# Performance work log

Hardware: AMD Instinct MI355X
Metric: run time of the kernel (lower is better)

The kernel has to match this reference:

```python
import jax, jax.numpy as jnp
import numpy as np

K = 10          # n_near
BN_EPS = 1e-5   # BatchNorm eps; running stats at init: mean=0, var=1


def knn_idx(xt, k):
    # xt: [b, n, c] -> [b, n, k] indices of k nearest (incl. self)
    sq = jnp.sum(xt * xt, axis=-1)                               # [b, n]
    d = sq[:, :, None] - 2.0 * jnp.einsum('bnc,bmc->bnm', xt, xt) + sq[:, None, :]
    return jax.lax.top_k(-d, k)[1]                               # [b, n, k]


def graph_feature(x, k):
    # x: [b, c, n] -> [b, 2c, n, k]  (DGCNN edge features)
    xt = x.transpose(0, 2, 1)                                    # [b, n, c]
    idx = knn_idx(xt, k)                                         # [b, n, k]
    nei = jnp.take_along_axis(xt[:, None, :, :], idx[..., None], axis=2)  # [b, n, k, c]
    cen = xt[:, :, None, :]                                      # [b, n, 1, c]
    feat = jnp.concatenate([nei - cen, jnp.broadcast_to(cen, nei.shape)], axis=-1)
    return feat.transpose(0, 3, 1, 2)                            # [b, 2c, n, k]


def conv_bn_act(x, w, b, g, t):
    # 1x1 conv (any spatial rank) + inference BatchNorm (mean=0, var=1) + GELU
    sh = (1, -1) + (1,) * (x.ndim - 2)
    y = jnp.einsum('oi,bi...->bo...', w, x) + b.reshape(sh)
    y = y * (g.reshape(sh) / jnp.sqrt(1.0 + BN_EPS)) + t.reshape(sh)
    return jax.nn.gelu(y)


def setup_inputs() -> dict:
    key = jax.random.key(0)
    ks = jax.random.split(key, 8)
    d = {'x': jax.random.normal(ks[0], (8, 64, 2048), jnp.float32)}
    dims = {'11': (152, 128), '12': (181, 152), '21': (430, 362),
            '22': (512, 430), '31': (595, 693), '32': (512, 595)}
    for i, (tag, (o, inp)) in enumerate(dims.items()):
        d['w' + tag] = jax.random.normal(jax.random.fold_in(key, i + 1), (o, inp), jnp.float32) * 0.02
        d['b' + tag] = jnp.zeros((o,), jnp.float32)
        d['g' + tag] = jnp.ones((o,), jnp.float32)
        d['t' + tag] = jnp.zeros((o,), jnp.float32)
    return d


def reference(x, w11, b11, g11, t11, w12, b12, g12, t12,
              w21, b21, g21, t21, w22, b22, g22, t22,
              w31, b31, g31, t31, w32, b32, g32, t32):
    f = graph_feature(x, K)                       # [b, 128, n, k]
    f = conv_bn_act(f, w11, b11, g11, t11)
    f = conv_bn_act(f, w12, b12, g12, t12)        # [b, 181, n, k]
    x1 = jnp.max(f, axis=-1)                      # [b, 181, n]
    f = graph_feature(x1, K)                      # [b, 362, n, k]
    f = conv_bn_act(f, w21, b21, g21, t21)
    f = conv_bn_act(f, w22, b22, g22, t22)        # [b, 512, n, k]
    x2 = jnp.max(f, axis=-1)                      # [b, 512, n]
    f = jnp.concatenate([x1, x2], axis=1)         # [b, 693, n]
    f = conv_bn_act(f, w31, b31, g31, t31)
    f = conv_bn_act(f, w32, b32, g32, t32)        # [b, 512, n]
    return f
```

## Files before the change

kernel.cpp:

```cpp
#include <hip/hip_runtime.h>


typedef float f4 __attribute__((ext_vector_type(4)));
typedef float f32x4 __attribute__((ext_vector_type(4)));
typedef short bf16x8 __attribute__((ext_vector_type(8)));

#define BNRSQ 0.9999950000374997f

__device__ __forceinline__ float gelu_f(float x){
  float a = 0.7978845608028654f * (x + 0.044715f * x * x * x);
  float e = __expf(2.0f * a);
  float t = 1.0f - 2.0f / (e + 1.0f);
  return 0.5f * x * (1.0f + t);
}

__device__ __forceinline__ short f2b(float x){
  unsigned u = __float_as_uint(x);
  unsigned r = (u + 0x7fffu + ((u >> 16) & 1u)) >> 16;
  return (short)r;
}
__device__ __forceinline__ float b2f(short s){
  return __uint_as_float(((unsigned)(unsigned short)s) << 16);
}

__global__ void makewt_k(const float* __restrict__ W, float* __restrict__ dst,
                         int O, int Cin, int Cpad, int ld, int split){
  int id = blockIdx.x * 256 + threadIdx.x;
  if (id >= Cpad * O) return;
  int c = id / O;
  int o = id - c * O;
  float v = 0.f;
  if (c < Cin){
    float w0 = W[(size_t)o * ld + c];
    v = split ? (W[(size_t)o * ld + Cin + c] - w0) : w0;
  }
  dst[id] = v;
}

__global__ void makew12r_k(const float* __restrict__ w12, float* __restrict__ Wr){
  int id = blockIdx.x * 256 + threadIdx.x;
  if (id >= 38 * 192 * 4) return;
  int i = id & 3;
  int c = (id >> 2) % 192;
  int kq = id / 768;
  int k = kq * 4 + i;
  float v = 0.f;
  if (c < 181 && k < 152) v = w12[(size_t)c * 152 + k];
  Wr[id] = v;
}

__global__ void makewsb_k(const float* __restrict__ W, short* __restrict__ dst){
  int n = blockIdx.x;
  int k = threadIdx.x;
  if (k >= 192) return;
  short v = 0;
  if (k < 181){
    if (n < 430) v = f2b(W[(size_t)n * 362 + k]);
    else if (n >= 448 && n < 878){
      int m = n - 448;
      v = f2b(W[(size_t)m * 362 + 181 + k] - W[(size_t)m * 362 + k]);
    }
  }
  dst[(size_t)n * 192 + k] = v;
}

__global__ void makewb_k(const float* __restrict__ W, short* __restrict__ dst,
                         int N, int K, int Kpad){
  int n = blockIdx.y;
  int k = blockIdx.x * 256 + threadIdx.x;
  if (k >= Kpad) return;
  short v = 0;
  if (n < N && k < K) v = f2b(W[(size_t)n * K + k]);
  dst[(size_t)n * Kpad + k] = v;
}

__global__ __launch_bounds__(256) void transpose_k(const float* __restrict__ x, float* __restrict__ xt){
  __shared__ float tile[64][65];
  int b = blockIdx.y;
  int n0 = blockIdx.x * 64;
  int t = threadIdx.x;
  int a = t & 63, r = t >> 6;
  #pragma unroll
  for (int s = 0; s < 16; s++){
    int c = r + s * 4;
    tile[c][a] = x[((size_t)b * 64 + c) * 2048 + n0 + a];
  }
  __syncthreads();
  #pragma unroll
  for (int s = 0; s < 16; s++){
    int n = r + s * 4;
    xt[((size_t)b * 2048 + n0 + n) * 64 + a] = tile[a][n];
  }
}

__global__ __launch_bounds__(256) void sqnorm_k(const float* __restrict__ X, float* __restrict__ sq,
                                                int C, int ld, int npts){
  int gid = blockIdx.x * blockDim.x + threadIdx.x;
  int wid = gid >> 6, lane = gid & 63;
  if (wid >= npts) return;
  const float* row = X + (size_t)wid * ld;
  float s = 0.f;
  for (int c = lane; c < C; c += 64){ float v = row[c]; s += v * v; }
  #pragma unroll
  for (int off = 32; off; off >>= 1) s += __shfl_xor(s, off);
  if (lane == 0) sq[wid] = s;
}

__global__ __launch_bounds__(256) void dist_k(const float* __restrict__ X, const float* __restrict__ sq,
                                              float* __restrict__ dist, int C, int ldx){
  __shared__ float As[16][132];
  __shared__ float Bs[16][132];
  const int z = blockIdx.z;
  const float* Xb = X + (size_t)z * 2048 * ldx;
  const float* sqb = sq + (z << 11);
  float* db = dist + (size_t)z * 2048 * 2048;
  const int i0 = blockIdx.y * 128, j0 = blockIdx.x * 128;
  const int t = threadIdx.x;
  const int ti = t >> 4, tj = t & 15;
  const int r = t & 127, q8 = (t >> 7) * 8;
  float acc[2][2][4][4];
  #pragma unroll
  for (int a = 0; a < 2; a++)
    #pragma unroll
    for (int b = 0; b < 2; b++)
      #pragma unroll
      for (int u = 0; u < 4; u++)
        #pragma unroll
        for (int v = 0; v < 4; v++) acc[a][b][u][v] = 0.f;
  const float* Ag = Xb + (size_t)(i0 + r) * ldx + q8;
  const float* Bg = Xb + (size_t)(j0 + r) * ldx + q8;
  for (int c0 = 0; c0 < C; c0 += 16){
    f4 av0 = *(const f4*)(Ag + c0);
    f4 av1 = *(const f4*)(Ag + c0 + 4);
    f4 bv0 = *(const f4*)(Bg + c0);
    f4 bv1 = *(const f4*)(Bg + c0 + 4);
    __syncthreads();
    #pragma unroll
    for (int i = 0; i < 4; i++){
      As[q8 + i][r] = av0[i];  As[q8 + 4 + i][r] = av1[i];
      Bs[q8 + i][r] = bv0[i];  Bs[q8 + 4 + i][r] = bv1[i];
    }
    __syncthreads();
    #pragma unroll
    for (int k = 0; k < 16; k++){
      f4 a0 = *(const f4*)&As[k][ti * 4];
      f4 a1 = *(const f4*)&As[k][ti * 4 + 64];
      f4 b0 = *(const f4*)&Bs[k][tj * 4];
      f4 b1 = *(const f4*)&Bs[k][tj * 4 + 64];
      #pragma unroll
      for (int u = 0; u < 4; u++)
        #pragma unroll
        for (int v = 0; v < 4; v++){
          acc[0][0][u][v] += a0[u] * b0[v];
          acc[0][1][u][v] += a0[u] * b1[v];
          acc[1][0][u][v] += a1[u] * b0[v];
          acc[1][1][u][v] += a1[u] * b1[v];
        }
    }
  }
  #pragma unroll
  for (int ia = 0; ia < 2; ia++){
    #pragma unroll
    for (int u = 0; u < 4; u++){
      int i = i0 + ia * 64 + ti * 4 + u;
      float si = sqb[i];
      #pragma unroll
      for (int jb = 0; jb < 2; jb++){
        int j = j0 + jb * 64 + tj * 4;
        f4 o;
        #pragma unroll
        for (int v = 0; v < 4; v++) o[v] = si + sqb[j + v] - 2.0f * acc[ia][jb][u][v];
        *(f4*)&db[(size_t)i * 2048 + j] = o;
      }
    }
  }
}

__global__ __launch_bounds__(256) void topk_k(const float* __restrict__ dist, int* __restrict__ idxout){
  int z = blockIdx.y;
  int lane = threadIdx.x & 63;
  int row = blockIdx.x * 4 + (threadIdx.x >> 6);
  const float* d = dist + (size_t)z * 2048 * 2048 + (size_t)row * 2048;
  float v[32];
  #pragma unroll
  for (int s = 0; s < 32; s++) v[s] = d[s * 64 + lane];
  int* outp = idxout + (size_t)z * 20480 + (size_t)row * 10;
  for (int it = 0; it < 10; ++it){
    float bv = 3.0e38f; int bi = 0x7fffffff;
    #pragma unroll
    for (int s = 0; s < 32; s++){
      if (v[s] < bv){ bv = v[s]; bi = s * 64 + lane; }
    }
    #pragma unroll
    for (int off = 32; off; off >>= 1){
      float ov = __shfl_xor(bv, off);
      int   oi = __shfl_xor(bi, off);
      if (ov < bv || (ov == bv && oi < bi)){ bv = ov; bi = oi; }
    }
    #pragma unroll
    for (int s = 0; s < 32; s++) if (s * 64 + lane == bi) v[s] = 3.0e38f;
    if (lane == 0) outp[it] = bi;
  }
}

__global__ __launch_bounds__(256) void yz_k(const float* __restrict__ Amat, int C,
                                            const float* __restrict__ B1, const float* __restrict__ B2,
                                            int O, float* __restrict__ Y, float* __restrict__ Z){
  __shared__ float As[16][68];
  __shared__ float B1s[16][68];
  __shared__ float B2s[16][68];
  int m0 = blockIdx.y * 64, o0 = blockIdx.x * 64;
  int t = threadIdx.x;
  int cc = t & 15, rr = t >> 4;
  int oo = t & 63, kk = t >> 6;
  float accY[4][4], accZ[4][4];
  #pragma unroll
  for (int u = 0; u < 4; u++)
    #pragma unroll
    for (int v = 0; v < 4; v++){ accY[u][v] = 0.f; accZ[u][v] = 0.f; }
  for (int c0 = 0; c0 < C; c0 += 16){
    #pragma unroll
    for (int u = 0; u < 4; u++){
      int ii = rr + u * 16;
      As[cc][ii] = ((c0 + cc) < C) ? Amat[(size_t)(m0 + ii) * C + c0 + cc] : 0.f;
    }
    #pragma unroll
    for (int u = 0; u < 4; u++){
      int c = kk * 4 + u;
      bool ok = ((c0 + c) < C) && ((o0 + oo) < O);
      B1s[c][oo] = ok ? B1[(size_t)(c0 + c) * O + o0 + oo] : 0.f;
      B2s[c][oo] = ok ? B2[(size_t)(c0 + c) * O + o0 + oo] : 0.f;
    }
    __syncthreads();
    #pragma unroll
    for (int k = 0; k < 16; k++){
      f4 a  = *(const f4*)&As[k][rr * 4];
      f4 b1 = *(const f4*)&B1s[k][cc * 4];
      f4 b2 = *(const f4*)&B2s[k][cc * 4];
      #pragma unroll
      for (int u = 0; u < 4; u++)
        #pragma unroll
        for (int v = 0; v < 4; v++){
          accY[u][v] += a[u] * b1[v];
          accZ[u][v] += a[u] * b2[v];
        }
    }
    __syncthreads();
  }
  #pragma unroll
  for (int u = 0; u < 4; u++){
    int m = m0 + rr * 4 + u;
    #pragma unroll
    for (int v = 0; v < 4; v++){
      int o = o0 + cc * 4 + v;
      if (o < O){
        Y[(size_t)m * O + o] = accY[u][v];
        Z[(size_t)m * O + o] = accZ[u][v];
      }
    }
  }
}

__global__ __launch_bounds__(256) void fused1_k(
    const float* __restrict__ Y1, const float* __restrict__ Z1,
    const int* __restrict__ idx, const float* __restrict__ Wr12,
    const float* __restrict__ bb11, const float* __restrict__ gg11, const float* __restrict__ tt11,
    const float* __restrict__ bb12, const float* __restrict__ gg12, const float* __restrict__ tt12,
    float* __restrict__ x1t){
  __shared__ float h1[80][152];
  __shared__ int sidx[80];
  const int n0 = blockIdx.x * 8;
  const int t = threadIdx.x;
  if (t < 80) sidx[t] = idx[(size_t)n0 * 10 + t];
  __syncthreads();
  const int base = (n0 >> 11) << 11;
  {
    const int tc = t & 63, tr = t >> 6;
    for (int c = tc; c < 152; c += 64){
      float bb = bb11[c], sc = gg11[c] * BNRSQ, tb = tt11[c];
      for (int r = tr; r < 80; r += 4){
        int p = r / 10;
        int j = base + sidx[r];
        float y = Y1[(size_t)j * 152 + c] + Z1[(size_t)(n0 + p) * 152 + c];
        h1[r][c] = gelu_f((y + bb) * sc + tb);
      }
    }
  }
  __syncthreads();
  const int p = t >> 5, kh = (t >> 4) & 1, cg = t & 15;
  const int rbase = p * 10 + kh * 5;
  #pragma unroll 1
  for (int jh = 0; jh < 2; jh++){
    float acc[5][6];
    #pragma unroll
    for (int k = 0; k < 5; k++)
      #pragma unroll
      for (int j = 0; j < 6; j++) acc[k][j] = 0.f;
    for (int kq = 0; kq < 38; kq++){
      const float* wp = Wr12 + ((size_t)kq * 192 + cg) * 4 + jh * 6 * 64;
      f4 wv[6];
      #pragma unroll
      for (int j = 0; j < 6; j++) wv[j] = *(const f4*)(wp + j * 64);
      f4 hv[5];
      #pragma unroll
      for (int k = 0; k < 5; k++) hv[k] = *(const f4*)&h1[rbase + k][kq * 4];
      #pragma unroll
      for (int k = 0; k < 5; k++)
        #pragma unroll
        for (int j = 0; j < 6; j++)
          acc[k][j] += hv[k][0] * wv[j][0] + hv[k][1] * wv[j][1]
                     + hv[k][2] * wv[j][2] + hv[k][3] * wv[j][3];
    }
    #pragma unroll
    for (int j = 0; j < 6; j++){
      int c = cg + (jh * 6 + j) * 16;
      float m = 0.f;
      if (c < 181){
        float bb = bb12[c], sc = gg12[c] * BNRSQ, tb = tt12[c];
        m = -3.0e38f;
        #pragma unroll
        for (int k = 0; k < 5; k++){
          float v = gelu_f((acc[k][j] + bb) * sc + tb);
          m = fmaxf(m, v);
        }
      }
      float o = __shfl_xor(m, 16);
      m = fmaxf(m, o);
      if (kh == 0) x1t[(size_t)(n0 + p) * 192 + c] = (c < 181) ? m : 0.f;
    }
  }
}

__global__ __launch_bounds__(256) void castx1_k(const float* __restrict__ x1t, short* __restrict__ x1b){
  int id = blockIdx.x * 256 + threadIdx.x;
  f4 v = *(const f4*)&x1t[(size_t)id * 4];
  short4 o;
  o.x = f2b(v[0]); o.y = f2b(v[1]); o.z = f2b(v[2]); o.w = f2b(v[3]);
  *(short4*)&x1b[(size_t)id * 4] = o;
}

__global__ __launch_bounds__(256) void h2_k(
    const float* __restrict__ YZ, const int* __restrict__ idx,
    const float* __restrict__ bb21, const float* __restrict__ gg21, const float* __restrict__ tt21,
    short* __restrict__ H2){
  __shared__ int sidx[10];
  int bl = blockIdx.x;
  int t = threadIdx.x;
  if (t < 10) sidx[t] = ((bl >> 11) << 11) + idx[(size_t)bl * 10 + t];
  __syncthreads();
  int cA = t;
  int cB = t + 256;
  float zA = YZ[(size_t)bl * 896 + 448 + cA] + bb21[cA];
  float scA = gg21[cA] * BNRSQ, tbA = tt21[cA];
  float zB = 0.f, scB = 0.f, tbB = 0.f;
  bool realB = cB < 430, padB = cB < 448;
  if (realB){
    zB = YZ[(size_t)bl * 896 + 448 + cB] + bb21[cB];
    scB = gg21[cB] * BNRSQ; tbB = tt21[cB];
  }
  #pragma unroll
  for (int k = 0; k < 10; k++){
    int nb = sidx[k];
    size_t rb = ((size_t)bl * 10 + k) * 448;
    float yA = YZ[(size_t)nb * 896 + cA] + zA;
    H2[rb + cA] = f2b(gelu_f(yA * scA + tbA));
    if (padB){
      short v = 0;
      if (realB){
        float yB = YZ[(size_t)nb * 896 + cB] + zB;
        v = f2b(gelu_f(yB * scB + tbB));
      }
      H2[rb + cB] = v;
    }
  }
}

template<int MODE>
__global__ __launch_bounds__(256) void gemm_k(const short* __restrict__ A,
                                              const short* __restrict__ Bt,
                                              int Kp, int Nld, int Nreal,
                                              const float* __restrict__ bv,
                                              const float* __restrict__ gv,
                                              const float* __restrict__ tv,
                                              void* __restrict__ outp){
  __shared__ short As[128][40];
  __shared__ short Bs[128][40];
  const int t = threadIdx.x;
  const int w = t >> 6, l = t & 63;
  const int m0 = blockIdx.y * 128, n0 = blockIdx.x * 128;
  f32x4 acc[2][8];
  #pragma unroll
  for (int i = 0; i < 2; i++)
    #pragma unroll
    for (int j = 0; j < 8; j++) acc[i][j] = (f32x4)0.f;
  const int ar = t >> 2, akc = t & 3;
  const short* Ag0 = A + (size_t)(m0 + ar) * Kp + akc * 8;
  const short* Ag1 = A + (size_t)(m0 + 64 + ar) * Kp + akc * 8;
  const short* Bg0 = Bt + (size_t)(n0 + ar) * Kp + akc * 8;
  const short* Bg1 = Bt + (size_t)(n0 + 64 + ar) * Kp + akc * 8;
  const int mrow = w * 32 + (l & 15);
  const int kg = (l >> 4) * 8;
  const int cl = l & 15;
  for (int k0 = 0; k0 < Kp; k0 += 32){
    int4 va0 = *(const int4*)(Ag0 + k0);
    int4 va1 = *(const int4*)(Ag1 + k0);
    int4 vb0 = *(const int4*)(Bg0 + k0);
    int4 vb1 = *(const int4*)(Bg1 + k0);
    __syncthreads();
    *(int4*)&As[ar][akc * 8]      = va0;
    *(int4*)&As[ar + 64][akc * 8] = va1;
    *(int4*)&Bs[ar][akc * 8]      = vb0;
    *(int4*)&Bs[ar + 64][akc * 8] = vb1;
    __syncthreads();
    bf16x8 a0 = *(const bf16x8*)&As[mrow][kg];
    bf16x8 a1 = *(const bf16x8*)&As[mrow + 16][kg];
    #pragma unroll
    for (int ni = 0; ni < 8; ni++){
      bf16x8 b = *(const bf16x8*)&Bs[cl + ni * 16][kg];
      acc[0][ni] = __builtin_amdgcn_mfma_f32_16x16x32_bf16(a0, b, acc[0][ni], 0, 0, 0);
      acc[1][ni] = __builtin_amdgcn_mfma_f32_16x16x32_bf16(a1, b, acc[1][ni], 0, 0, 0);
    }
  }
  const int rbase = (l >> 4) * 4;
  #pragma unroll
  for (int ni = 0; ni < 8; ni++){
    int n = n0 + ni * 16 + cl;
    float bb = 0.f, sc = 0.f, tb = 0.f;
    if (MODE != 2 && n < Nreal){ bb = bv[n]; sc = gv[n] * BNRSQ; tb = tv[n]; }
    #pragma unroll
    for (int mi = 0; mi < 2; mi++){
      #pragma unroll
      for (int r = 0; r < 4; r++){
        int m = m0 + w * 32 + mi * 16 + rbase + r;
        float a = acc[mi][ni][r];
        float v = (MODE == 2) ? a : gelu_f((a + bb) * sc + tb);
        if (MODE == 0) ((short*)outp)[(size_t)m * Nld + n] = f2b(v);
        else           ((float*)outp)[(size_t)m * Nld + n] = v;
      }
    }
  }
}

__global__ __launch_bounds__(256) void kmax_k(const short* __restrict__ Pb, short* __restrict__ x2b){
  int p = blockIdx.x;
  int t = threadIdx.x;
  #pragma unroll
  for (int j = 0; j < 2; j++){
    int o = t + j * 256;
    float m = -3.0e38f;
    #pragma unroll
    for (int k = 0; k < 10; k++) m = fmaxf(m, b2f(Pb[((size_t)p * 10 + k) * 512 + o]));
    x2b[(size_t)p * 512 + o] = f2b(m);
  }
}

__global__ __launch_bounds__(256) void fcat_k(const float* __restrict__ x1t, const short* __restrict__ x2b,
                                              short* __restrict__ F){
  size_t g = blockIdx.x;
  int t = threadIdx.x;
  for (int c = t; c < 704; c += 256){
    short v = 0;
    if (c < 181) v = f2b(x1t[g * 192 + c]);
    else if (c < 693) v = x2b[g * 512 + (c - 181)];
    F[g * 704 + c] = v;
  }
}

__global__ __launch_bounds__(256) void trout_k(const float* __restrict__ H6, float* __restrict__ out){
  __shared__ float tile[64][65];
  int b = blockIdx.z;
  int nc = blockIdx.x * 64, oc = blockIdx.y * 64;
  int t = threadIdx.x;
  int a = t & 63, r = t >> 6;
  #pragma unroll
  for (int s = 0; s < 16; s++){
    int nl = r + s * 4;
    tile[nl][a] = H6[((size_t)b * 2048 + nc + nl) * 512 + oc + a];
  }
  __syncthreads();
  #pragma unroll
  for (int s = 0; s < 16; s++){
    int ol = r + s * 4;
    out[((size_t)(b * 512 + oc + ol)) * 2048 + nc + a] = tile[a][ol];
  }
}

extern "C" void kernel_launch(void* const* d_in, const int* in_sizes, int n_in,
                              void* d_out, int out_size, void* d_ws, size_t ws_size,
                              hipStream_t stream) {
  const float* x   = (const float*)d_in[0];
  const float* w11 = (const float*)d_in[1];
  const float* b11 = (const float*)d_in[2];
  const float* g11 = (const float*)d_in[3];
  const float* t11 = (const float*)d_in[4];
  const float* w12 = (const float*)d_in[5];
  const float* b12 = (const float*)d_in[6];
  const float* g12 = (const float*)d_in[7];
  const float* t12 = (const float*)d_in[8];
  const float* w21 = (const float*)d_in[9];
  const float* b21 = (const float*)d_in[10];
  const float* g21 = (const float*)d_in[11];
  const float* t21 = (const float*)d_in[12];
  const float* w22 = (const float*)d_in[13];
  const float* b22 = (const float*)d_in[14];
  const float* g22 = (const float*)d_in[15];
  const float* t22 = (const float*)d_in[16];
  const float* w31 = (const float*)d_in[17];
  const float* b31 = (const float*)d_in[18];
  const float* g31 = (const float*)d_in[19];
  const float* t31 = (const float*)d_in[20];
  const float* w32 = (const float*)d_in[21];
  const float* b32 = (const float*)d_in[22];
  const float* g32 = (const float*)d_in[23];
  const float* t32 = (const float*)d_in[24];
  float* out = (float*)d_out;
  char* ws = (char*)d_ws;

  size_t off = 0;
  auto alloc = [&](size_t nbytes) -> char* {
    char* p = ws + off;
    off += ((nbytes + 255) & ~(size_t)255);
    return p;
  };
  float* x1t  = (float*)alloc((size_t)16384 * 192 * 4);
  short* x1b  = (short*)alloc((size_t)16384 * 192 * 2);
  short* x2b  = (short*)alloc((size_t)16384 * 512 * 2);
  float* sq1  = (float*)alloc(65536);
  float* sq2  = (float*)alloc(65536);
  int*   idx1 = (int*)  alloc(655360);
  int*   idx2 = (int*)  alloc(655360);
  float* WaT11 = (float*)alloc(64 * 152 * 4);
  float* WdT11 = (float*)alloc(64 * 152 * 4);
  float* Wr12  = (float*)alloc(38 * 192 * 4 * 4);
  short* W21sb = (short*)alloc((size_t)896 * 192 * 2);
  short* W22b  = (short*)alloc((size_t)512 * 448 * 2);
  short* W31b  = (short*)alloc((size_t)640 * 704 * 2);
  short* W32b  = (short*)alloc((size_t)512 * 640 * 2);
  char* arena = ws + off;
  const size_t ARENA = 93323264;
  if (off + ARENA > ws_size) return;
  float* distP = (float*)(arena);
  float* Y1    = (float*)(arena + 67108864);
  float* Z1    = (float*)(arena + 77070336);
  float* xt    = (float*)(arena + 87031808);
  short* Pb    = (short*)(arena);
  short* H2b   = (short*)(arena + 41943040);
  float* YZ2g  = (float*)(arena + 78643200);
  short* F     = (short*)(arena);
  short* H5    = (short*)(arena + 23068672);
  float* H6    = (float*)(arena + 44040192);

  auto mk = [&](const float* W, float* dst, int O, int Cin, int Cpad, int ld, int split){
    int n = Cpad * O;
    makewt_k<<<dim3((n + 255) / 256), dim3(256), 0, stream>>>(W, dst, O, Cin, Cpad, ld, split);
  };
  mk(w11, WaT11, 152, 64, 64, 128, 0);
  mk(w11, WdT11, 152, 64, 64, 128, 1);
  makew12r_k<<<dim3(114), dim3(256), 0, stream>>>(w12, Wr12);
  makewsb_k<<<dim3(896), dim3(256), 0, stream>>>(w21, W21sb);
  makewb_k<<<dim3(2, 512), dim3(256), 0, stream>>>(w22, W22b, 512, 430, 448);
  makewb_k<<<dim3(3, 640), dim3(256), 0, stream>>>(w31, W31b, 595, 693, 704);
  makewb_k<<<dim3(3, 512), dim3(256), 0, stream>>>(w32, W32b, 512, 595, 640);

  transpose_k<<<dim3(32, 8), dim3(256), 0, stream>>>(x, xt);
  sqnorm_k<<<dim3(4096), dim3(256), 0, stream>>>(xt, sq1, 64, 64, 16384);

  for (int pb = 0; pb < 2; pb++){
    dist_k<<<dim3(16, 16, 4), dim3(256), 0, stream>>>(xt + (size_t)pb * 4 * 2048 * 64,
                                                      sq1 + pb * 8192, distP, 64, 64);
    topk_k<<<dim3(512, 4), dim3(256), 0, stream>>>(distP, idx1 + (size_t)pb * 4 * 20480);
  }
  yz_k<<<dim3(3, 256), dim3(256), 0, stream>>>(xt, 64, WaT11, WdT11, 152, Y1, Z1);
  fused1_k<<<dim3(2048), dim3(256), 0, stream>>>(Y1, Z1, idx1, Wr12,
                                                 b11, g11, t11, b12, g12, t12, x1t);
  castx1_k<<<dim3(3072), dim3(256), 0, stream>>>(x1t, x1b);
  sqnorm_k<<<dim3(4096), dim3(256), 0, stream>>>(x1t, sq2, 192, 192, 16384);

  for (int pb = 0; pb < 2; pb++){
    dist_k<<<dim3(16, 16, 4), dim3(256), 0, stream>>>(x1t + (size_t)pb * 4 * 2048 * 192,
                                                      sq2 + pb * 8192, distP, 192, 192);
    topk_k<<<dim3(512, 4), dim3(256), 0, stream>>>(distP, idx2 + (size_t)pb * 4 * 20480);
  }
  for (int g = 0; g < 4; g++){
    gemm_k<2><<<dim3(7, 32), dim3(256), 0, stream>>>(x1b + (size_t)g * 4096 * 192, W21sb,
                                                     192, 896, 896,
                                                     nullptr, nullptr, nullptr, (void*)YZ2g);
    h2_k<<<dim3(4096), dim3(256), 0, stream>>>(YZ2g, idx2 + (size_t)g * 40960,
                                               b21, g21, t21, H2b);
    gemm_k<0><<<dim3(4, 320), dim3(256), 0, stream>>>(H2b, W22b, 448, 512, 512,
                                                      b22, g22, t22, (void*)Pb);
    kmax_k<<<dim3(4096), dim3(256), 0, stream>>>(Pb, x2b + (size_t)g * 4096 * 512);
  }

  fcat_k<<<dim3(16384), dim3(256), 0, stream>>>(x1t, x2b, F);
  gemm_k<0><<<dim3(5, 128), dim3(256), 0, stream>>>(F, W31b, 704, 640, 595,
                                                    b31, g31, t31, (void*)H5);
  gemm_k<1><<<dim3(4, 128), dim3(256), 0, stream>>>(H5, W32b, 640, 512, 512,
                                                    b32, g32, t32, (void*)H6);
  trout_k<<<dim3(32, 8, 8), dim3(256), 0, stream>>>(H6, out);
}
```

Measured before the change: 1.112 ms.

## Fuse neighbor gather+GELU into conv22 GEMM and fold cast/sqnorm into fused1

Removes the h2_k kernel and its materialized bf16 H2 buffer. The conv22 GEMM now gathers Y/Z rows by kNN index, applies the layer-21 bias/BN/GELU in registers, and writes bf16 straight into LDS. fused1_k is restructured to handle 4 points per block with 32-wide channel groups, and now also emits the bf16 copy of x1 and its squared norms. This drops the castx1 and sqnorm launches. In exchange, the GEMM A-tile loads become scattered fp32 gathers with per-element GELU recomputed for each output-column tile, which adds ALU work and irregular memory traffic.

```diff
diff --git a/kernel.cpp b/kernel.cpp
--- a/kernel.cpp
+++ b/kernel.cpp
@@ -72,6 +72,15 @@
   short v = 0;
   if (n < N && k < K) v = f2b(W[(size_t)n * K + k]);
   dst[(size_t)n * Kpad + k] = v;
+}
+
+__global__ void makebnp_k(const float* __restrict__ b21, const float* __restrict__ g21,
+                          const float* __restrict__ t21, float* __restrict__ bnp){
+  int c = blockIdx.x * 256 + threadIdx.x;
+  if (c >= 448) return;
+  float bb = 0.f, sc = 0.f, tb = 0.f;
+  if (c < 430){ bb = b21[c]; sc = g21[c] * BNRSQ; tb = t21[c]; }
+  bnp[c] = bb; bnp[448 + c] = sc; bnp[896 + c] = tb;
 }
 
 __global__ __launch_bounds__(256) void transpose_k(const float* __restrict__ x, float* __restrict__ xt){
@@ -266,19 +275,19 @@
     const int* __restrict__ idx, const float* __restrict__ Wr12,
     const float* __restrict__ bb11, const float* __restrict__ gg11, const float* __restrict__ tt11,
     const float* __restrict__ bb12, const float* __restrict__ gg12, const float* __restrict__ tt12,
-    float* __restrict__ x1t){
-  __shared__ float h1[80][152];
-  __shared__ int sidx[80];
-  const int n0 = blockIdx.x * 8;
+    float* __restrict__ x1t, short* __restrict__ x1b, float* __restrict__ sq2){
+  __shared__ float h1[40][152];
+  __shared__ int sidx[40];
+  const int n0 = blockIdx.x * 4;
   const int t = threadIdx.x;
-  if (t < 80) sidx[t] = idx[(size_t)n0 * 10 + t];
+  if (t < 40) sidx[t] = idx[(size_t)n0 * 10 + t];
   __syncthreads();
   const int base = (n0 >> 11) << 11;
   {
     const int tc = t & 63, tr = t >> 6;
     for (int c = tc; c < 152; c += 64){
       float bb = bb11[c], sc = gg11[c] * BNRSQ, tb = tt11[c];
-      for (int r = tr; r < 80; r += 4){
+      for (int r = tr; r < 40; r += 4){
         int p = r / 10;
         int j = base + sidx[r];
         float y = Y1[(size_t)j * 152 + c] + Z1[(size_t)(n0 + p) * 152 + c];
@@ -287,92 +296,54 @@
     }
   }
   __syncthreads();
-  const int p = t >> 5, kh = (t >> 4) & 1, cg = t & 15;
+  const int p = t >> 6, kh = (t >> 5) & 1, cg = t & 31;
   const int rbase = p * 10 + kh * 5;
-  #pragma unroll 1
-  for (int jh = 0; jh < 2; jh++){
-    float acc[5][6];
+  float acc[5][6];
+  #pragma unroll
+  for (int k = 0; k < 5; k++)
+    #pragma unroll
+    for (int j = 0; j < 6; j++) acc[k][j] = 0.f;
+  for (int kq = 0; kq < 38; kq++){
+    const float* wp = Wr12 + ((size_t)kq * 192 + cg) * 4;
+    f4 wv[6];
+    #pragma unroll
+    for (int j = 0; j < 6; j++) wv[j] = *(const f4*)(wp + j * 128);
+    f4 hv[5];
+    #pragma unroll
+    for (int k = 0; k < 5; k++) hv[k] = *(const f4*)&h1[rbase + k][kq * 4];
     #pragma unroll
     for (int k = 0; k < 5; k++)
       #pragma unroll
-      for (int j = 0; j < 6; j++) acc[k][j] = 0.f;
-    for (int kq = 0; kq < 38; kq++){
-      const float* wp = Wr12 + ((size_t)kq * 192 + cg) * 4 + jh * 6 * 64;
-      f4 wv[6];
-      #pragma unroll
-      for (int j = 0; j < 6; j++) wv[j] = *(const f4*)(wp + j * 64);
-      f4 hv[5];
-      #pragma unroll
-      for (int k = 0; k < 5; k++) hv[k] = *(const f4*)&h1[rbase + k][kq * 4];
-      #pragma unroll
-      for (int k = 0; k < 5; k++)
-        #pragma unroll
-        for (int j = 0; j < 6; j++)
-          acc[k][j] += hv[k][0] * wv[j][0] + hv[k][1] * wv[j][1]
-                     + hv[k][2] * wv[j][2] + hv[k][3] * wv[j][3];
-    }
-    #pragma unroll
-    for (int j = 0; j < 6; j++){
-      int c = cg + (jh * 6 + j) * 16;
-      float m = 0.f;
-      if (c < 181){
-        float bb = bb12[c], sc = gg12[c] * BNRSQ, tb = tt12[c];
-        m = -3.0e38f;
-        #pragma unroll
-        for (int k = 0; k < 5; k++){
-          float v = gelu_f((acc[k][j] + bb) * sc + tb);
-          m = fmaxf(m, v);
-        }
+      for (int j = 0; j < 6; j++)
+        acc[k][j] += hv[k][0] * wv[j][0] + hv[k][1] * wv[j][1]
+                   + hv[k][2] * wv[j][2] + hv[k][3] * wv[j][3];
+  }
+  float ssum = 0.f;
+  #pragma unroll
+  for (int j = 0; j < 6; j++){
+    int c = cg + j * 32;
+    float m = 0.f;
+    if (c < 181){
+      float bb = bb12[c], sc = gg12[c] * BNRSQ, tb = tt12[c];
+      m = -3.0e38f;
+      #pragma unroll
+      for (int k = 0; k < 5; k++){
+        float v = gelu_f((acc[k][j] + bb) * sc + tb);
+        m = fmaxf(m, v);
       }
-      float o = __shfl_xor(m, 16);
-      m = fmaxf(m, o);
-      if (kh == 0) x1t[(size_t)(n0 + p) * 192 + c] = (c < 181) ? m : 0.f;
-    }
-  }
-}
-
-__global__ __launch_bounds__(256) void castx1_k(const float* __restrict__ x1t, short* __restrict__ x1b){
-  int id = blockIdx.x * 256 + threadIdx.x;
-  f4 v = *(const f4*)&x1t[(size_t)id * 4];
-  short4 o;
-  o.x = f2b(v[0]); o.y = f2b(v[1]); o.z = f2b(v[2]); o.w = f2b(v[3]);
-  *(short4*)&x1b[(size_t)id * 4] = o;
-}
-
-__global__ __launch_bounds__(256) void h2_k(
-    const float* __restrict__ YZ, const int* __restrict__ idx,
-    const float* __restrict__ bb21, const float* __restrict__ gg21, const float* __restrict__ tt21,
-    short* __restrict__ H2){
-  __shared__ int sidx[10];
-  int bl = blockIdx.x;
-  int t = threadIdx.x;
-  if (t < 10) sidx[t] = ((bl >> 11) << 11) + idx[(size_t)bl * 10 + t];
-  __syncthreads();
-  int cA = t;
-  int cB = t + 256;
-  float zA = YZ[(size_t)bl * 896 + 448 + cA] + bb21[cA];
-  float scA = gg21[cA] * BNRSQ, tbA = tt21[cA];
-  float zB = 0.f, scB = 0.f, tbB = 0.f;
-  bool realB = cB < 430, padB = cB < 448;
-  if (realB){
-    zB = YZ[(size_t)bl * 896 + 448 + cB] + bb21[cB];
-    scB = gg21[cB] * BNRSQ; tbB = tt21[cB];
-  }
-  #pragma unroll
-  for (int k = 0; k < 10; k++){
-    int nb = sidx[k];
-    size_t rb = ((size_t)bl * 10 + k) * 448;
-    float yA = YZ[(size_t)nb * 896 + cA] + zA;
-    H2[rb + cA] = f2b(gelu_f(yA * scA + tbA));
-    if (padB){
-      short v = 0;
-      if (realB){
-        float yB = YZ[(size_t)nb * 896 + cB] + zB;
-        v = f2b(gelu_f(yB * scB + tbB));
-      }
-      H2[rb + cB] = v;
-    }
-  }
+    }
+    float o = __shfl_xor(m, 32);
+    m = fmaxf(m, o);
+    if (kh == 0){
+      float mv = (c < 181) ? m : 0.f;
+      x1t[(size_t)(n0 + p) * 192 + c] = mv;
+      x1b[(size_t)(n0 + p) * 192 + c] = f2b(mv);
+      ssum += mv * mv;
+    }
+  }
+  #pragma unroll
+  for (int off = 16; off; off >>= 1) ssum += __shfl_xor(ssum, off);
+  if (kh == 0 && cg == 0) sq2[n0 + p] = ssum;
 }
 
 template<int MODE>
@@ -436,6 +407,86 @@
         float v = (MODE == 2) ? a : gelu_f((a + bb) * sc + tb);
         if (MODE == 0) ((short*)outp)[(size_t)m * Nld + n] = f2b(v);
         else           ((float*)outp)[(size_t)m * Nld + n] = v;
+      }
+    }
+  }
+}
+
+__global__ __launch_bounds__(256) void gemm22f_k(
+    const float* __restrict__ YZ, const int* __restrict__ idx,
+    const short* __restrict__ Bt, const float* __restrict__ bnp,
+    const float* __restrict__ bv, const float* __restrict__ gv, const float* __restrict__ tv,
+    short* __restrict__ Pb){
+  __shared__ short As[128][40];
+  __shared__ short Bs[128][40];
+  const int t = threadIdx.x;
+  const int w = t >> 6, l = t & 63;
+  const int m0 = blockIdx.y * 128, n0 = blockIdx.x * 128;
+  f32x4 acc[2][8];
+  #pragma unroll
+  for (int i = 0; i < 2; i++)
+    #pragma unroll
+    for (int j = 0; j < 8; j++) acc[i][j] = (f32x4)0.f;
+  const int ar = t >> 2, akc = t & 3;
+  const int r0 = m0 + ar, r1 = m0 + 64 + ar;
+  const int p0 = r0 / 10, p1 = r1 / 10;
+  const int nb0 = ((p0 >> 11) << 11) + idx[r0];
+  const int nb1 = ((p1 >> 11) << 11) + idx[r1];
+  const float* y0p = YZ + (size_t)nb0 * 896;
+  const float* z0p = YZ + (size_t)p0 * 896 + 448;
+  const float* y1p = YZ + (size_t)nb1 * 896;
+  const float* z1p = YZ + (size_t)p1 * 896 + 448;
+  const short* Bg0 = Bt + (size_t)(n0 + ar) * 448 + akc * 8;
+  const short* Bg1 = Bt + (size_t)(n0 + 64 + ar) * 448 + akc * 8;
+  const int mrow = w * 32 + (l & 15);
+  const int kg = (l >> 4) * 8;
+  const int cl = l & 15;
+  for (int k0 = 0; k0 < 448; k0 += 32){
+    const int cb = k0 + akc * 8;
+    f4 bb0 = *(const f4*)(bnp + cb),       bb1 = *(const f4*)(bnp + cb + 4);
+    f4 sc0 = *(const f4*)(bnp + 448 + cb), sc1 = *(const f4*)(bnp + 448 + cb + 4);
+    f4 tb0 = *(const f4*)(bnp + 896 + cb), tb1 = *(const f4*)(bnp + 896 + cb + 4);
+    f4 ya0 = *(const f4*)(y0p + cb), ya1 = *(const f4*)(y0p + cb + 4);
+    f4 za0 = *(const f4*)(z0p + cb), za1 = *(const f4*)(z0p + cb + 4);
+    f4 yb0 = *(const f4*)(y1p + cb), yb1 = *(const f4*)(y1p + cb + 4);
+    f4 zb0 = *(const f4*)(z1p + cb), zb1 = *(const f4*)(z1p + cb + 4);
+    int4 vb0 = *(const int4*)(Bg0 + k0);
+    int4 vb1 = *(const int4*)(Bg1 + k0);
+    bf16x8 ha, hb;
+    #pragma unroll
+    for (int i = 0; i < 4; i++){
+      ha[i]     = f2b(gelu_f((ya0[i] + (za0[i] + bb0[i])) * sc0[i] + tb0[i]));
+      ha[4 + i] = f2b(gelu_f((ya1[i] + (za1[i] + bb1[i])) * sc1[i] + tb1[i]));
+      hb[i]     = f2b(gelu_f((yb0[i] + (zb0[i] + bb0[i])) * sc0[i] + tb0[i]));
+      hb[4 + i] = f2b(gelu_f((yb1[i] + (zb1[i] + bb1[i])) * sc1[i] + tb1[i]));
+    }
+    __syncthreads();
+    *(bf16x8*)&As[ar][akc * 8]      = ha;
+    *(bf16x8*)&As[ar + 64][akc * 8] = hb;
+    *(int4*)&Bs[ar][akc * 8]        = vb0;
+    *(int4*)&Bs[ar + 64][akc * 8]   = vb1;
+    __syncthreads();
+    bf16x8 a0 = *(const bf16x8*)&As[mrow][kg];
+    bf16x8 a1 = *(const bf16x8*)&As[mrow + 16][kg];
+    #pragma unroll
+    for (int ni = 0; ni < 8; ni++){
+      bf16x8 b = *(const bf16x8*)&Bs[cl + ni * 16][kg];
+      acc[0][ni] = __builtin_amdgcn_mfma_f32_16x16x32_bf16(a0, b, acc[0][ni], 0, 0, 0);
+      acc[1][ni] = __builtin_amdgcn_mfma_f32_16x16x32_bf16(a1, b, acc[1][ni], 0, 0, 0);
+    }
+  }
+  const int rb = (l >> 4) * 4;
+  #pragma unroll
+  for (int ni = 0; ni < 8; ni++){
+    int n = n0 + ni * 16 + cl;
+    float bb = bv[n], sc = gv[n] * BNRSQ, tb = tv[n];
+    #pragma unroll
+    for (int mi = 0; mi < 2; mi++){
+      #pragma unroll
+      for (int r = 0; r < 4; r++){
+        int m = m0 + w * 32 + mi * 16 + rb + r;
+        float v = gelu_f((acc[mi][ni][r] + bb) * sc + tb);
+        Pb[(size_t)m * 512 + n] = f2b(v);
       }
     }
   }
@@ -536,6 +587,7 @@
   short* W22b  = (short*)alloc((size_t)512 * 448 * 2);
   short* W31b  = (short*)alloc((size_t)640 * 704 * 2);
   short* W32b  = (short*)alloc((size_t)512 * 640 * 2);
+  float* bnp   = (float*)alloc(1344 * 4);
   char* arena = ws + off;
   const size_t ARENA = 93323264;
   if (off + ARENA > ws_size) return;
@@ -544,8 +596,7 @@
   float* Z1    = (float*)(arena + 77070336);
   float* xt    = (float*)(arena + 87031808);
   short* Pb    = (short*)(arena);
-  short* H2b   = (short*)(arena + 41943040);
-  float* YZ2g  = (float*)(arena + 78643200);
+  float* YZ2g  = (float*)(arena + 41943040);
   short* F     = (short*)(arena);
   short* H5    = (short*)(arena + 23068672);
   float* H6    = (float*)(arena + 44040192);
@@ -561,6 +612,7 @@
   makewb_k<<<dim3(2, 512), dim3(256), 0, stream>>>(w22, W22b, 512, 430, 448);
   makewb_k<<<dim3(3, 640), dim3(256), 0, stream>>>(w31, W31b, 595, 693, 704);
   makewb_k<<<dim3(3, 512), dim3(256), 0, stream>>>(w32, W32b, 512, 595, 640);
+  makebnp_k<<<dim3(2), dim3(256), 0, stream>>>(b21, g21, t21, bnp);
 
   transpose_k<<<dim3(32, 8), dim3(256), 0, stream>>>(x, xt);
   sqnorm_k<<<dim3(4096), dim3(256), 0, stream>>>(xt, sq1, 64, 64, 16384);
@@ -571,10 +623,9 @@
     topk_k<<<dim3(512, 4), dim3(256), 0, stream>>>(distP, idx1 + (size_t)pb * 4 * 20480);
   }
   yz_k<<<dim3(3, 256), dim3(256), 0, stream>>>(xt, 64, WaT11, WdT11, 152, Y1, Z1);
-  fused1_k<<<dim3(2048), dim3(256), 0, stream>>>(Y1, Z1, idx1, Wr12,
-                                                 b11, g11, t11, b12, g12, t12, x1t);
-  castx1_k<<<dim3(3072), dim3(256), 0, stream>>>(x1t, x1b);
-  sqnorm_k<<<dim3(4096), dim3(256), 0, stream>>>(x1t, sq2, 192, 192, 16384);
+  fused1_k<<<dim3(4096), dim3(256), 0, stream>>>(Y1, Z1, idx1, Wr12,
+                                                 b11, g11, t11, b12, g12, t12,
+                                                 x1t, x1b, sq2);
 
   for (int pb = 0; pb < 2; pb++){
     dist_k<<<dim3(16, 16, 4), dim3(256), 0, stream>>>(x1t + (size_t)pb * 4 * 2048 * 192,
@@ -585,10 +636,8 @@
     gemm_k<2><<<dim3(7, 32), dim3(256), 0, stream>>>(x1b + (size_t)g * 4096 * 192, W21sb,
                                                      192, 896, 896,
                                                      nullptr, nullptr, nullptr, (void*)YZ2g);
-    h2_k<<<dim3(4096), dim3(256), 0, stream>>>(YZ2g, idx2 + (size_t)g * 40960,
-                                               b21, g21, t21, H2b);
-    gemm_k<0><<<dim3(4, 320), dim3(256), 0, stream>>>(H2b, W22b, 448, 512, 512,
-                                                      b22, g22, t22, (void*)Pb);
+    gemm22f_k<<<dim3(4, 320), dim3(256), 0, stream>>>(YZ2g, idx2 + (size_t)g * 40960,
+                                                      W22b, bnp, b22, g22, t22, Pb);
     kmax_k<<<dim3(4096), dim3(256), 0, stream>>>(Pb, x2b + (size_t)g * 4096 * 512);
   }
 
```

Measured after the change: 1.225 ms. +10.2%, slower.
